# Kernel optimization log

Hardware: AMD Instinct MI355X
Metric: run time of the kernel (lower is better)

The kernel has to match this reference:

```python
import jax, jax.numpy as jnp
import numpy as np

N = 40000      # option nodes
E = 320000     # edges per edge type (avg in-degree 8)
NT = 3         # edge types
L = 3          # message-passing layers
D = 128        # node_dim
HID = 256      # hidden_dim
H = 4          # attention heads
C = HID // H   # per-head channels


def _ln(x, g, b):
    m = x.mean(-1, keepdims=True)
    v = ((x - m) ** 2).mean(-1, keepdims=True)
    return g * (x - m) * jax.lax.rsqrt(v + 1e-5) + b


def _gelu(x):
    return jax.nn.gelu(x, approximate=False)  # torch default = exact erf GELU


def _gat(h, src, dst, W, a_src, a_dst, bias):
    # PyG GATConv: shared src/dst linear, add_self_loops=False, eval (no dropout)
    xp = (h @ W).reshape(N, H, C)                      # (N,H,C)
    e = jax.nn.leaky_relu((xp * a_src).sum(-1)[src] + (xp * a_dst).sum(-1)[dst], 0.2)  # (E,H)
    emax = jax.ops.segment_max(e, dst, num_segments=N)
    emax = jnp.where(jnp.isfinite(emax), emax, 0.0)    # nodes with no in-edges
    ex = jnp.exp(e - emax[dst])
    den = jax.ops.segment_sum(ex, dst, num_segments=N)
    alpha = ex / (den[dst] + 1e-16)                    # segment softmax over incoming edges
    out = jax.ops.segment_sum(alpha[:, :, None] * xp[src], dst, num_segments=N)
    return out.reshape(N, HID) + bias


def _glorot(key, shape):
    fan_in = shape[-2] if len(shape) > 1 else shape[-1]
    return jax.random.normal(key, shape, jnp.float32) / np.sqrt(fan_in)


def setup_inputs() -> dict:
    key = jax.random.key(0)
    ks = jax.random.split(key, 16)
    return {
        "x": jax.random.normal(ks[0], (N, D), jnp.float32),
        "liquidity_features": jax.random.normal(ks[1], (N, 4), jnp.float32),
        "edge_index": jax.random.randint(ks[2], (NT, 2, E), 0, N, jnp.int32),
        "edge_weight": jax.random.uniform(ks[3], (NT, E), jnp.float32),
        "in_W": _glorot(ks[4], (D, HID)), "in_b": jnp.zeros((HID,)),
        "in_g": jnp.ones((HID,)), "in_bb": jnp.zeros((HID,)),
        "gat_W": _glorot(ks[5], (L, NT, HID, HID)),
        "gat_asrc": _glorot(ks[6], (L, NT, H, C)) * 0.1,
        "gat_adst": _glorot(ks[7], (L, NT, H, C)) * 0.1,
        "gat_bias": jnp.zeros((L, NT, HID)),
        "ln_g": jnp.ones((L, HID)), "ln_b": jnp.zeros((L, HID)),
        "gate_W": _glorot(ks[8], (HID + 4, 1)), "gate_b": jnp.zeros((1,)),
        "out_W1": _glorot(ks[9], (HID, HID)), "out_b1": jnp.zeros((HID,)),
        "out_g": jnp.ones((HID,)), "out_bb": jnp.zeros((HID,)),
        "out_W2": _glorot(ks[10], (HID, D)), "out_b2": jnp.zeros((D,)),
        "ro_W1": _glorot(ks[11], (D, HID)), "ro_b1": jnp.zeros((HID,)),
        "ro_W2": _glorot(ks[12], (HID, HID)), "ro_b2": jnp.zeros((HID,)),
    }


def reference(x, liquidity_features, edge_index, edge_weight, in_W, in_b, in_g, in_bb,
              gat_W, gat_asrc, gat_adst, gat_bias, ln_g, ln_b, gate_W, gate_b,
              out_W1, out_b1, out_g, out_bb, out_W2, out_b2,
              ro_W1, ro_b1, ro_W2, ro_b2):
    h = _gelu(_ln(x @ in_W + in_b, in_g, in_bb))  # input_proj
    # incoming edge-weight gate (static graph -> identical every layer)
    wsum = jnp.zeros((N,), x.dtype)
    deg = jnp.zeros((N,), x.dtype)
    for t in range(NT):
        dst = edge_index[t, 1]
        wsum = wsum.at[dst].add(edge_weight[t])
        deg = deg.at[dst].add(1.0)
    ewg = (0.5 + jax.nn.sigmoid(wsum / jnp.maximum(deg, 1.0)))[:, None]  # (N,1)
    layer_outputs = []
    for i in range(L):
        agg = jnp.zeros((N, HID), x.dtype)  # HeteroConv aggr='sum'
        for t in range(NT):
            agg = agg + _gat(h, edge_index[t, 0], edge_index[t, 1],
                             gat_W[i, t], gat_asrc[i, t], gat_adst[i, t], gat_bias[i, t])
        gate = jax.nn.sigmoid(jnp.concatenate([agg, liquidity_features], -1) @ gate_W + gate_b)
        hn = (gate * agg + (1.0 - gate) * h) * ewg   # liquidity gate + edge-weight gate
        h = _gelu(_ln(hn + h, ln_g[i], ln_b[i]))     # residual + LayerNorm + GELU
        layer_outputs.append(h)
    ho = _gelu(_ln(h @ out_W1 + out_b1, out_g, out_bb)) @ out_W2 + out_b2  # (N,D)
    surf = _gelu(ho.mean(0) @ ro_W1 + ro_b1) @ ro_W2 + ro_b2               # (HID,)
    return (ho, surf, *layer_outputs)
```

## Files before the change

kernel.cpp:

```cpp
#include <hip/hip_runtime.h>
#include <hip/hip_bf16.h>
#include <math.h>

#define NN 40000
#define EE 320000
#define NT 3
#define LL 3
#define DD 128
#define HID 256
#define NH 4
#define CC 64
#define NP 768

typedef __attribute__((ext_vector_type(8))) short short8;
typedef __attribute__((ext_vector_type(4))) float f32x4;

__device__ __forceinline__ float gelu_f(float x) {
    return 0.5f * x * (1.0f + erff(x * 0.70710678118654752440f));
}
__device__ __forceinline__ float lrelu_f(float x) {
    return x > 0.0f ? x : 0.2f * x;
}
__device__ __forceinline__ float bf2f(unsigned short u) {
    unsigned int x = ((unsigned int)u) << 16;
    float f;
    __builtin_memcpy(&f, &x, 4);
    return f;
}
__device__ __forceinline__ unsigned short f2bf(float f) {
    __hip_bfloat16 h = __float2bfloat16(f);
    unsigned short u;
    __builtin_memcpy(&u, &h, 2);
    return u;
}
__device__ __forceinline__ void gload16(const void* g, void* l) {
    __builtin_amdgcn_global_load_lds(
        (const __attribute__((address_space(1))) unsigned int*)g,
        (__attribute__((address_space(3))) unsigned int*)l, 16, 0, 0);
}

__global__ void wconv_k(const float* __restrict__ W, unsigned short* __restrict__ Wt,
                        int nmat, int K, int N) {
    int idx = blockIdx.x * 256 + threadIdx.x;
    int tot = nmat * K * N;
    if (idx >= tot) return;
    int m = idx / (K * N);
    int rem = idx - m * (K * N);
    int k = rem / N;
    int n = rem - k * N;
    Wt[(size_t)m * K * N + (size_t)n * K + k] = f2bf(W[idx]);
}

__global__ void xconv_k(const float* __restrict__ x, unsigned short* __restrict__ xb) {
    int idx = blockIdx.x * 256 + threadIdx.x;
    if (idx >= NN * DD / 4) return;
    float4 v = *reinterpret_cast<const float4*>(&x[(size_t)idx * 4]);
    ushort4 o;
    o.x = f2bf(v.x); o.y = f2bf(v.y); o.z = f2bf(v.z); o.w = f2bf(v.w);
    *reinterpret_cast<ushort4*>(&xb[(size_t)idx * 4]) = o;
}

__global__ __launch_bounds__(256) void gemm_mfma_k(const unsigned short* __restrict__ A,
                                                   const unsigned short* __restrict__ Bt,
                                                   const float* __restrict__ bias,
                                                   float* __restrict__ Cf,
                                                   unsigned short* __restrict__ Cb,
                                                   int M, int K, int N) {
    __shared__ __align__(16) short As[128 * 32];
    __shared__ __align__(16) short Bs[128 * 32];
    int bm = blockIdx.y * 128, bn = blockIdx.x * 128;
    int tid = threadIdx.x;
    int lane = tid & 63, w = tid >> 6;
    int wr = w >> 1, wc = w & 1;
    int l16 = lane & 15, kgrp = lane >> 4;
    f32x4 acc[4][4] = {};
    for (int k0 = 0; k0 < K; k0 += 32) {
        #pragma unroll
        for (int i = 0; i < 2; i++) {
            int chunk = (i * 4 + w) * 64 + lane;
            int row = chunk >> 2, kq = chunk & 3;
            int grow = bm + row; if (grow > M - 1) grow = M - 1;
            gload16(A + (size_t)grow * K + k0 + kq * 8, &As[(i * 4 + w) * 512]);
        }
        #pragma unroll
        for (int i = 0; i < 2; i++) {
            int chunk = (i * 4 + w) * 64 + lane;
            int row = chunk >> 2, kq = chunk & 3;
            gload16(Bt + (size_t)(bn + row) * K + k0 + kq * 8, &Bs[(i * 4 + w) * 512]);
        }
        __syncthreads();
        short8 af[4], bf[4];
        #pragma unroll
        for (int mi = 0; mi < 4; mi++) {
            int row = wr * 64 + mi * 16 + l16;
            af[mi] = *reinterpret_cast<const short8*>(&As[row * 32 + kgrp * 8]);
        }
        #pragma unroll
        for (int ni = 0; ni < 4; ni++) {
            int nrow = wc * 64 + ni * 16 + l16;
            bf[ni] = *reinterpret_cast<const short8*>(&Bs[nrow * 32 + kgrp * 8]);
        }
        #pragma unroll
        for (int mi = 0; mi < 4; mi++)
            #pragma unroll
            for (int ni = 0; ni < 4; ni++)
                acc[mi][ni] = __builtin_amdgcn_mfma_f32_16x16x32_bf16(af[mi], bf[ni], acc[mi][ni], 0, 0, 0);
        __syncthreads();
    }
    #pragma unroll
    for (int mi = 0; mi < 4; mi++) {
        #pragma unroll
        for (int r = 0; r < 4; r++) {
            int row = bm + wr * 64 + mi * 16 + (lane >> 4) * 4 + r;
            if (row < M) {
                #pragma unroll
                for (int ni = 0; ni < 4; ni++) {
                    int col = bn + wc * 64 + ni * 16 + l16;
                    float v = acc[mi][ni][r] + (bias ? bias[col] : 0.0f);
                    if (Cf) Cf[(size_t)row * N + col] = v;
                    if (Cb) Cb[(size_t)row * N + col] = f2bf(v);
                }
            }
        }
    }
}

__global__ __launch_bounds__(256) void ln_gelu_k(const float* __restrict__ y,
                                                 const float* __restrict__ g,
                                                 const float* __restrict__ b,
                                                 float* __restrict__ outf,
                                                 unsigned short* __restrict__ outb) {
    int n = blockIdx.x * 4 + (threadIdx.x >> 6);
    int lane = threadIdx.x & 63;
    float4 v = *reinterpret_cast<const float4*>(&y[(size_t)n * HID + lane * 4]);
    float s = v.x + v.y + v.z + v.w;
    float q = v.x * v.x + v.y * v.y + v.z * v.z + v.w * v.w;
    #pragma unroll
    for (int o = 32; o; o >>= 1) { s += __shfl_xor(s, o); q += __shfl_xor(q, o); }
    float mean = s * (1.0f / HID);
    float var = q * (1.0f / HID) - mean * mean;
    float rs = rsqrtf(var + 1e-5f);
    float4 gv = *reinterpret_cast<const float4*>(&g[lane * 4]);
    float4 bv = *reinterpret_cast<const float4*>(&b[lane * 4]);
    float o0 = gelu_f(gv.x * (v.x - mean) * rs + bv.x);
    float o1 = gelu_f(gv.y * (v.y - mean) * rs + bv.y);
    float o2 = gelu_f(gv.z * (v.z - mean) * rs + bv.z);
    float o3 = gelu_f(gv.w * (v.w - mean) * rs + bv.w);
    if (outf) {
        float4 ov = {o0, o1, o2, o3};
        *reinterpret_cast<float4*>(&outf[(size_t)n * HID + lane * 4]) = ov;
    }
    ushort4 ob;
    ob.x = f2bf(o0); ob.y = f2bf(o1); ob.z = f2bf(o2); ob.w = f2bf(o3);
    *reinterpret_cast<ushort4*>(&outb[(size_t)n * HID + lane * 4]) = ob;
}

__global__ void hist_k(const int* __restrict__ ei, int* __restrict__ cnt) {
    int gid = blockIdx.x * 256 + threadIdx.x;
    if (gid >= NT * EE) return;
    int t = gid / EE, e = gid - t * EE;
    int dst = ei[(size_t)t * 2 * EE + EE + e];
    atomicAdd(&cnt[t * NN + dst], 1);
}

__global__ __launch_bounds__(256) void scan1_k(const int* __restrict__ cnt, int* __restrict__ bsum, int n) {
    int i = blockIdx.x * 256 + threadIdx.x;
    int v = (i < n) ? cnt[i] : 0;
    #pragma unroll
    for (int o = 32; o; o >>= 1) v += __shfl_xor(v, o);
    __shared__ int s4[4];
    if ((threadIdx.x & 63) == 0) s4[threadIdx.x >> 6] = v;
    __syncthreads();
    if (threadIdx.x == 0) bsum[blockIdx.x] = s4[0] + s4[1] + s4[2] + s4[3];
}

__global__ __launch_bounds__(512) void scan2_k(const int* __restrict__ bsum, int* __restrict__ boff, int nb) {
    __shared__ int sh[512];
    int t = threadIdx.x;
    int v = (t < nb) ? bsum[t] : 0;
    sh[t] = v;
    __syncthreads();
    for (int o = 1; o < 512; o <<= 1) {
        int tv = (t >= o) ? sh[t - o] : 0;
        __syncthreads();
        sh[t] += tv;
        __syncthreads();
    }
    if (t < nb) boff[t] = sh[t] - v;
}

__global__ __launch_bounds__(256) void scan3_k(const int* __restrict__ cnt, const int* __restrict__ boff,
                                               int* __restrict__ roff, int n) {
    int i = blockIdx.x * 256 + threadIdx.x;
    int lane = threadIdx.x & 63, w = threadIdx.x >> 6;
    int v = (i < n) ? cnt[i] : 0;
    int s = v;
    #pragma unroll
    for (int o = 1; o < 64; o <<= 1) {
        int tv = __shfl_up(s, o);
        if (lane >= o) s += tv;
    }
    __shared__ int ws_[4];
    if (lane == 63) ws_[w] = s;
    __syncthreads();
    int add = 0;
    for (int k = 0; k < 4; k++) if (k < w) add += ws_[k];
    int incl = s + add + boff[blockIdx.x];
    if (i < n) roff[i] = incl - v;
    if (i == n - 1) roff[n] = incl;
}

__global__ void scatter_k(const int* __restrict__ ei, const float* __restrict__ ew,
                          const int* __restrict__ roff, int* __restrict__ cur,
                          int* __restrict__ csr_src, float* __restrict__ csr_ew) {
    int gid = blockIdx.x * 256 + threadIdx.x;
    if (gid >= NT * EE) return;
    int t = gid / EE, e = gid - t * EE;
    int src = ei[(size_t)t * 2 * EE + e];
    int dst = ei[(size_t)t * 2 * EE + EE + e];
    int pos = roff[t * NN + dst] + atomicAdd(&cur[t * NN + dst], 1);
    csr_src[pos] = src;
    csr_ew[pos] = ew[gid];
}

__global__ void ewg_kernel(const int* __restrict__ roff, const float* __restrict__ csr_ew,
                           float* __restrict__ ewg) {
    int n = blockIdx.x * 256 + threadIdx.x;
    if (n >= NN) return;
    float ws = 0.0f;
    int dg = 0;
    for (int t = 0; t < NT; t++) {
        int beg = roff[t * NN + n], end = roff[t * NN + n + 1];
        dg += end - beg;
        for (int e = beg; e < end; e++) ws += csr_ew[e];
    }
    float m = dg > 1 ? (float)dg : 1.0f;
    float z = ws / m;
    ewg[n] = 0.5f + 1.0f / (1.0f + __expf(-z));
}

__global__ __launch_bounds__(256) void compute_s_k(const unsigned short* __restrict__ xpa,
                                                   const float* __restrict__ asrc,
                                                   const float* __restrict__ adst,
                                                   float* __restrict__ ss,
                                                   float* __restrict__ sd) {
    int t = blockIdx.x / (NN / 4);
    int node = (blockIdx.x % (NN / 4)) * 4 + (threadIdx.x >> 6);
    int lane = threadIdx.x & 63;
    ushort4 v = *reinterpret_cast<const ushort4*>(&xpa[(size_t)node * NP + t * HID + lane * 4]);
    float4 av = *reinterpret_cast<const float4*>(&asrc[t * HID + lane * 4]);
    float4 dv = *reinterpret_cast<const float4*>(&adst[t * HID + lane * 4]);
    float x0 = bf2f(v.x), x1 = bf2f(v.y), x2 = bf2f(v.z), x3 = bf2f(v.w);
    float p = x0 * av.x + x1 * av.y + x2 * av.z + x3 * av.w;
    float q = x0 * dv.x + x1 * dv.y + x2 * dv.z + x3 * dv.w;
    #pragma unroll
    for (int o = 8; o; o >>= 1) { p += __shfl_xor(p, o); q += __shfl_xor(q, o); }
    if ((lane & 15) == 0) {
        ss[((size_t)t * NN + node) * NH + (lane >> 4)] = p;
        sd[((size_t)t * NN + node) * NH + (lane >> 4)] = q;
    }
}

__global__ __launch_bounds__(256) void layer_k(const unsigned short* __restrict__ xpa,
                                               const float* __restrict__ ss,
                                               const float* __restrict__ sd,
                                               const int* __restrict__ roff,
                                               const int* __restrict__ rsrc,
                                               const float* __restrict__ gatb,
                                               const float* __restrict__ hin,
                                               const float* __restrict__ liq,
                                               const float* __restrict__ gW,
                                               const float* __restrict__ gb,
                                               const float* __restrict__ ewg,
                                               const float* __restrict__ lg,
                                               const float* __restrict__ lb,
                                               float* __restrict__ hout,
                                               unsigned short* __restrict__ houtb) {
    int node = blockIdx.x * 4 + (threadIdx.x >> 6);
    int lane = threadIdx.x & 63;
    int h = lane >> 4;
    float agg0 = 0, agg1 = 0, agg2 = 0, agg3 = 0;
    #pragma unroll
    for (int t = 0; t < NT; t++) {
        int beg = roff[t * NN + node], end = roff[t * NN + node + 1];
        if (beg == end) continue;
        float sdh = sd[((size_t)t * NN + node) * NH + h];
        float m = -1e30f, den = 0, a0 = 0, a1 = 0, a2 = 0, a3 = 0;
        int s_n = rsrc[beg];
        float sv_n = ss[((size_t)t * NN + s_n) * NH + h];
        ushort4 xr_n = *reinterpret_cast<const ushort4*>(&xpa[(size_t)s_n * NP + t * HID + lane * 4]);
        for (int e = beg; e < end; e++) {
            float sv_c = sv_n;
            ushort4 xr_c = xr_n;
            if (e + 1 < end) {
                int sn = rsrc[e + 1];
                sv_n = ss[((size_t)t * NN + sn) * NH + h];
                xr_n = *reinterpret_cast<const ushort4*>(&xpa[(size_t)sn * NP + t * HID + lane * 4]);
            }
            float sc = lrelu_f(sv_c + sdh);
            float wg;
            if (sc > m) {
                float r = __expf(m - sc);
                den *= r; a0 *= r; a1 *= r; a2 *= r; a3 *= r;
                m = sc;
                wg = 1.0f;
            } else {
                wg = __expf(sc - m);
            }
            den += wg;
            a0 += wg * bf2f(xr_c.x);
            a1 += wg * bf2f(xr_c.y);
            a2 += wg * bf2f(xr_c.z);
            a3 += wg * bf2f(xr_c.w);
        }
        float inv = 1.0f / (den + 1e-16f);
        agg0 += a0 * inv; agg1 += a1 * inv; agg2 += a2 * inv; agg3 += a3 * inv;
    }
    float4 bb0 = *reinterpret_cast<const float4*>(&gatb[lane * 4]);
    float4 bb1 = *reinterpret_cast<const float4*>(&gatb[HID + lane * 4]);
    float4 bb2 = *reinterpret_cast<const float4*>(&gatb[2 * HID + lane * 4]);
    agg0 += bb0.x + bb1.x + bb2.x;
    agg1 += bb0.y + bb1.y + bb2.y;
    agg2 += bb0.z + bb1.z + bb2.z;
    agg3 += bb0.w + bb1.w + bb2.w;
    float4 gwv = *reinterpret_cast<const float4*>(&gW[lane * 4]);
    float part = agg0 * gwv.x + agg1 * gwv.y + agg2 * gwv.z + agg3 * gwv.w;
    if (lane < 4) part += liq[node * 4 + lane] * gW[HID + lane];
    #pragma unroll
    for (int o = 32; o; o >>= 1) part += __shfl_xor(part, o);
    float gate = 1.0f / (1.0f + __expf(-(part + gb[0])));
    float eg = ewg[node];
    float4 hh = *reinterpret_cast<const float4*>(&hin[(size_t)node * HID + lane * 4]);
    float v0 = (gate * agg0 + (1.0f - gate) * hh.x) * eg + hh.x;
    float v1 = (gate * agg1 + (1.0f - gate) * hh.y) * eg + hh.y;
    float v2 = (gate * agg2 + (1.0f - gate) * hh.z) * eg + hh.z;
    float v3 = (gate * agg3 + (1.0f - gate) * hh.w) * eg + hh.w;
    float s = v0 + v1 + v2 + v3;
    float q = v0 * v0 + v1 * v1 + v2 * v2 + v3 * v3;
    #pragma unroll
    for (int o = 32; o; o >>= 1) { s += __shfl_xor(s, o); q += __shfl_xor(q, o); }
    float mean = s * (1.0f / HID);
    float var = q * (1.0f / HID) - mean * mean;
    float rs = rsqrtf(var + 1e-5f);
    float4 lgv = *reinterpret_cast<const float4*>(&lg[lane * 4]);
    float4 lbv = *reinterpret_cast<const float4*>(&lb[lane * 4]);
    float o0 = gelu_f(lgv.x * (v0 - mean) * rs + lbv.x);
    float o1 = gelu_f(lgv.y * (v1 - mean) * rs + lbv.y);
    float o2 = gelu_f(lgv.z * (v2 - mean) * rs + lbv.z);
    float o3 = gelu_f(lgv.w * (v3 - mean) * rs + lbv.w);
    float4 ov = {o0, o1, o2, o3};
    *reinterpret_cast<float4*>(&hout[(size_t)node * HID + lane * 4]) = ov;
    ushort4 ob;
    ob.x = f2bf(o0); ob.y = f2bf(o1); ob.z = f2bf(o2); ob.w = f2bf(o3);
    *reinterpret_cast<ushort4*>(&houtb[(size_t)node * HID + lane * 4]) = ob;
}

__global__ __launch_bounds__(128) void colpart_k(const float* __restrict__ ho,
                                                 float* __restrict__ part) {
    int c = threadIdx.x, b = blockIdx.x;
    float s = 0.0f;
    for (int r = b; r < NN; r += 256) s += ho[(size_t)r * DD + c];
    part[b * DD + c] = s;
}

__global__ __launch_bounds__(256) void readout_k(const float* __restrict__ part,
                                                 const float* __restrict__ W1,
                                                 const float* __restrict__ b1,
                                                 const float* __restrict__ W2,
                                                 const float* __restrict__ b2,
                                                 float* __restrict__ surf) {
    __shared__ float m[DD];
    __shared__ float a1[HID];
    int t = threadIdx.x;
    if (t < DD) {
        float s = 0.0f;
        for (int b = 0; b < 256; b++) s += part[b * DD + t];
        m[t] = s / (float)NN;
    }
    __syncthreads();
    float s1 = b1[t];
    for (int k = 0; k < DD; k++) s1 += m[k] * W1[k * HID + t];
    a1[t] = gelu_f(s1);
    __syncthreads();
    float s2 = b2[t];
    for (int k = 0; k < HID; k++) s2 += a1[k] * W2[k * HID + t];
    surf[t] = s2;
}

extern "C" void kernel_launch(void* const* d_in, const int* in_sizes, int n_in,
                              void* d_out, int out_size, void* d_ws, size_t ws_size,
                              hipStream_t stream) {
    const float* x       = (const float*)d_in[0];
    const float* liq     = (const float*)d_in[1];
    const int*   ei      = (const int*)d_in[2];
    const float* ew      = (const float*)d_in[3];
    const float* in_W    = (const float*)d_in[4];
    const float* in_b    = (const float*)d_in[5];
    const float* in_g    = (const float*)d_in[6];
    const float* in_bb   = (const float*)d_in[7];
    const float* gat_W   = (const float*)d_in[8];
    const float* gat_as  = (const float*)d_in[9];
    const float* gat_ad  = (const float*)d_in[10];
    const float* gat_b   = (const float*)d_in[11];
    const float* ln_g    = (const float*)d_in[12];
    const float* ln_b    = (const float*)d_in[13];
    const float* gate_W  = (const float*)d_in[14];
    const float* gate_b  = (const float*)d_in[15];
    const float* out_W1  = (const float*)d_in[16];
    const float* out_b1  = (const float*)d_in[17];
    const float* out_g   = (const float*)d_in[18];
    const float* out_bb  = (const float*)d_in[19];
    const float* out_W2  = (const float*)d_in[20];
    const float* out_b2  = (const float*)d_in[21];
    const float* ro_W1   = (const float*)d_in[22];
    const float* ro_b1   = (const float*)d_in[23];
    const float* ro_W2   = (const float*)d_in[24];
    const float* ro_b2   = (const float*)d_in[25];

    float* out = (float*)d_out;
    float* out_ho   = out;
    float* out_surf = out + (size_t)NN * DD;
    float* out_h[3];
    out_h[0] = out_surf + HID;
    out_h[1] = out_h[0] + (size_t)NN * HID;
    out_h[2] = out_h[1] + (size_t)NN * HID;

    char* wsb = (char*)d_ws;
    size_t off = 0;
    auto alloc = [&](size_t bytes) { char* p = wsb + off; off += (bytes + 255) & ~(size_t)255; return p; };
    unsigned short* xpa = (unsigned short*)alloc((size_t)NN * NP * 2);
    float* Cf32 = (float*)xpa;
    unsigned short* xb = xpa + (size_t)NN * 512;
    unsigned short* hb = (unsigned short*)alloc((size_t)NN * HID * 2);
    unsigned short* Wt_in  = (unsigned short*)alloc((size_t)DD * HID * 2);
    unsigned short* Wt_gat = (unsigned short*)alloc((size_t)LL * NT * HID * HID * 2);
    unsigned short* Wt_o1  = (unsigned short*)alloc((size_t)HID * HID * 2);
    unsigned short* Wt_o2  = (unsigned short*)alloc((size_t)HID * DD * 2);
    size_t cew_b = (size_t)NT * EE * 4;
    size_t cnt_b = (size_t)NT * NN * 4;
    char* R = alloc(cew_b + cnt_b + 2 * 2048 * 4);
    float* cew = (float*)R;
    int* cnt   = (int*)(R + cew_b);
    int* bsum  = (int*)(R + cew_b + cnt_b);
    int* boff  = bsum + 2048;
    float* ss  = (float*)R;
    float* sd  = ss + (size_t)NT * NN * NH;
    int* roff  = (int*)alloc(((size_t)NT * NN + 1) * 4);
    int* rsrc  = (int*)alloc((size_t)NT * EE * 4);
    float* ewg = (float*)alloc((size_t)NN * 4);
    float* cpart = (float*)alloc((size_t)256 * DD * 4);

    const int NSC = (NT * NN + 255) / 256;

    wconv_k<<<(DD * HID + 255) / 256, 256, 0, stream>>>(in_W, Wt_in, 1, DD, HID);
    wconv_k<<<(LL * NT * HID * HID + 255) / 256, 256, 0, stream>>>(gat_W, Wt_gat, LL * NT, HID, HID);
    wconv_k<<<(HID * HID + 255) / 256, 256, 0, stream>>>(out_W1, Wt_o1, 1, HID, HID);
    wconv_k<<<(HID * DD + 255) / 256, 256, 0, stream>>>(out_W2, Wt_o2, 1, HID, DD);
    xconv_k<<<(NN * DD / 4 + 255) / 256, 256, 0, stream>>>(x, xb);

    gemm_mfma_k<<<dim3(HID / 128, (NN + 127) / 128), 256, 0, stream>>>(
        xb, Wt_in, in_b, Cf32, nullptr, NN, DD, HID);
    ln_gelu_k<<<NN / 4, 256, 0, stream>>>(Cf32, in_g, in_bb, out_h[0], hb);

    hipMemsetAsync(cnt, 0, cnt_b, stream);
    hist_k<<<(NT * EE + 255) / 256, 256, 0, stream>>>(ei, cnt);
    scan1_k<<<NSC, 256, 0, stream>>>(cnt, bsum, NT * NN);
    scan2_k<<<1, 512, 0, stream>>>(bsum, boff, NSC);
    scan3_k<<<NSC, 256, 0, stream>>>(cnt, boff, roff, NT * NN);
    hipMemsetAsync(cnt, 0, cnt_b, stream);
    scatter_k<<<(NT * EE + 255) / 256, 256, 0, stream>>>(ei, ew, roff, cnt, rsrc, cew);
    ewg_kernel<<<(NN + 255) / 256, 256, 0, stream>>>(roff, cew, ewg);

    const float* hin_f = out_h[0];
    for (int i = 0; i < LL; i++) {
        gemm_mfma_k<<<dim3(NP / 128, (NN + 127) / 128), 256, 0, stream>>>(
            hb, Wt_gat + (size_t)i * NP * HID, nullptr, nullptr, xpa, NN, HID, NP);
        compute_s_k<<<NT * (NN / 4), 256, 0, stream>>>(
            xpa, gat_as + (size_t)i * NT * HID, gat_ad + (size_t)i * NT * HID, ss, sd);
        layer_k<<<NN / 4, 256, 0, stream>>>(
            xpa, ss, sd, roff, rsrc, gat_b + (size_t)i * NT * HID,
            hin_f, liq, gate_W, gate_b, ewg, ln_g + i * HID, ln_b + i * HID,
            out_h[i], hb);
        hin_f = out_h[i];
    }

    gemm_mfma_k<<<dim3(HID / 128, (NN + 127) / 128), 256, 0, stream>>>(
        hb, Wt_o1, out_b1, Cf32, nullptr, NN, HID, HID);
    ln_gelu_k<<<NN / 4, 256, 0, stream>>>(Cf32, out_g, out_bb, nullptr, hb);
    gemm_mfma_k<<<dim3(DD / 128, (NN + 127) / 128), 256, 0, stream>>>(
        hb, Wt_o2, out_b2, out_ho, nullptr, NN, HID, DD);

    colpart_k<<<256, 128, 0, stream>>>(out_ho, cpart);
    readout_k<<<1, 256, 0, stream>>>(cpart, ro_W1, ro_b1, ro_W2, ro_b2, out_surf);
}
```

Before: 851.2 us.

## Persistent grid-stride layer kernel, drop online-softmax max, read residual from bf16

```diff
diff --git a/kernel.cpp b/kernel.cpp
--- a/kernel.cpp
+++ b/kernel.cpp
@@ -11,6 +11,7 @@
 #define NH 4
 #define CC 64
 #define NP 768
+#define LGRID 2048
 
 typedef __attribute__((ext_vector_type(8))) short short8;
 typedef __attribute__((ext_vector_type(4))) float f32x4;
@@ -267,7 +268,6 @@
                                                const int* __restrict__ roff,
                                                const int* __restrict__ rsrc,
                                                const float* __restrict__ gatb,
-                                               const float* __restrict__ hin,
                                                const float* __restrict__ liq,
                                                const float* __restrict__ gW,
                                                const float* __restrict__ gb,
@@ -275,84 +275,83 @@
                                                const float* __restrict__ lg,
                                                const float* __restrict__ lb,
                                                float* __restrict__ hout,
-                                               unsigned short* __restrict__ houtb) {
-    int node = blockIdx.x * 4 + (threadIdx.x >> 6);
+                                               unsigned short* __restrict__ hb) {
+    int wid = blockIdx.x * 4 + (threadIdx.x >> 6);
     int lane = threadIdx.x & 63;
     int h = lane >> 4;
-    float agg0 = 0, agg1 = 0, agg2 = 0, agg3 = 0;
-    #pragma unroll
-    for (int t = 0; t < NT; t++) {
-        int beg = roff[t * NN + node], end = roff[t * NN + node + 1];
-        if (beg == end) continue;
-        float sdh = sd[((size_t)t * NN + node) * NH + h];
-        float m = -1e30f, den = 0, a0 = 0, a1 = 0, a2 = 0, a3 = 0;
-        int s_n = rsrc[beg];
-        float sv_n = ss[((size_t)t * NN + s_n) * NH + h];
-        ushort4 xr_n = *reinterpret_cast<const ushort4*>(&xpa[(size_t)s_n * NP + t * HID + lane * 4]);
-        for (int e = beg; e < end; e++) {
-            float sv_c = sv_n;
-            ushort4 xr_c = xr_n;
-            if (e + 1 < end) {
-                int sn = rsrc[e + 1];
-                sv_n = ss[((size_t)t * NN + sn) * NH + h];
-                xr_n = *reinterpret_cast<const ushort4*>(&xpa[(size_t)sn * NP + t * HID + lane * 4]);
-            }
-            float sc = lrelu_f(sv_c + sdh);
-            float wg;
-            if (sc > m) {
-                float r = __expf(m - sc);
-                den *= r; a0 *= r; a1 *= r; a2 *= r; a3 *= r;
-                m = sc;
-                wg = 1.0f;
-            } else {
-                wg = __expf(sc - m);
-            }
-            den += wg;
-            a0 += wg * bf2f(xr_c.x);
-            a1 += wg * bf2f(xr_c.y);
-            a2 += wg * bf2f(xr_c.z);
-            a3 += wg * bf2f(xr_c.w);
-        }
-        float inv = 1.0f / (den + 1e-16f);
-        agg0 += a0 * inv; agg1 += a1 * inv; agg2 += a2 * inv; agg3 += a3 * inv;
-    }
+    const int nw = LGRID * 4;
     float4 bb0 = *reinterpret_cast<const float4*>(&gatb[lane * 4]);
     float4 bb1 = *reinterpret_cast<const float4*>(&gatb[HID + lane * 4]);
     float4 bb2 = *reinterpret_cast<const float4*>(&gatb[2 * HID + lane * 4]);
-    agg0 += bb0.x + bb1.x + bb2.x;
-    agg1 += bb0.y + bb1.y + bb2.y;
-    agg2 += bb0.z + bb1.z + bb2.z;
-    agg3 += bb0.w + bb1.w + bb2.w;
+    float bs0 = bb0.x + bb1.x + bb2.x;
+    float bs1 = bb0.y + bb1.y + bb2.y;
+    float bs2 = bb0.z + bb1.z + bb2.z;
+    float bs3 = bb0.w + bb1.w + bb2.w;
     float4 gwv = *reinterpret_cast<const float4*>(&gW[lane * 4]);
-    float part = agg0 * gwv.x + agg1 * gwv.y + agg2 * gwv.z + agg3 * gwv.w;
-    if (lane < 4) part += liq[node * 4 + lane] * gW[HID + lane];
-    #pragma unroll
-    for (int o = 32; o; o >>= 1) part += __shfl_xor(part, o);
-    float gate = 1.0f / (1.0f + __expf(-(part + gb[0])));
-    float eg = ewg[node];
-    float4 hh = *reinterpret_cast<const float4*>(&hin[(size_t)node * HID + lane * 4]);
-    float v0 = (gate * agg0 + (1.0f - gate) * hh.x) * eg + hh.x;
-    float v1 = (gate * agg1 + (1.0f - gate) * hh.y) * eg + hh.y;
-    float v2 = (gate * agg2 + (1.0f - gate) * hh.z) * eg + hh.z;
-    float v3 = (gate * agg3 + (1.0f - gate) * hh.w) * eg + hh.w;
-    float s = v0 + v1 + v2 + v3;
-    float q = v0 * v0 + v1 * v1 + v2 * v2 + v3 * v3;
-    #pragma unroll
-    for (int o = 32; o; o >>= 1) { s += __shfl_xor(s, o); q += __shfl_xor(q, o); }
-    float mean = s * (1.0f / HID);
-    float var = q * (1.0f / HID) - mean * mean;
-    float rs = rsqrtf(var + 1e-5f);
+    float gwl = (lane < 4) ? gW[HID + lane] : 0.0f;
+    float gb0 = gb[0];
     float4 lgv = *reinterpret_cast<const float4*>(&lg[lane * 4]);
     float4 lbv = *reinterpret_cast<const float4*>(&lb[lane * 4]);
-    float o0 = gelu_f(lgv.x * (v0 - mean) * rs + lbv.x);
-    float o1 = gelu_f(lgv.y * (v1 - mean) * rs + lbv.y);
-    float o2 = gelu_f(lgv.z * (v2 - mean) * rs + lbv.z);
-    float o3 = gelu_f(lgv.w * (v3 - mean) * rs + lbv.w);
-    float4 ov = {o0, o1, o2, o3};
-    *reinterpret_cast<float4*>(&hout[(size_t)node * HID + lane * 4]) = ov;
-    ushort4 ob;
-    ob.x = f2bf(o0); ob.y = f2bf(o1); ob.z = f2bf(o2); ob.w = f2bf(o3);
-    *reinterpret_cast<ushort4*>(&houtb[(size_t)node * HID + lane * 4]) = ob;
+
+    for (int node = wid; node < NN; node += nw) {
+        float agg0 = 0, agg1 = 0, agg2 = 0, agg3 = 0;
+        #pragma unroll
+        for (int t = 0; t < NT; t++) {
+            int base = t * NN;
+            int beg = roff[base + node], end = roff[base + node + 1];
+            if (beg == end) continue;
+            float sdh = sd[(size_t)(base + node) * NH + h];
+            float den = 0, a0 = 0, a1 = 0, a2 = 0, a3 = 0;
+            int sp = rsrc[beg];
+            float svp = ss[(size_t)(base + sp) * NH + h];
+            ushort4 xrp = *reinterpret_cast<const ushort4*>(&xpa[(size_t)sp * NP + t * HID + lane * 4]);
+            for (int e = beg; e < end; e++) {
+                float sv_c = svp;
+                ushort4 xr_c = xrp;
+                int en = (e + 1 < end) ? (e + 1) : e;
+                int sn = rsrc[en];
+                svp = ss[(size_t)(base + sn) * NH + h];
+                xrp = *reinterpret_cast<const ushort4*>(&xpa[(size_t)sn * NP + t * HID + lane * 4]);
+                float wg = __expf(lrelu_f(sv_c + sdh));
+                den += wg;
+                a0 += wg * bf2f(xr_c.x);
+                a1 += wg * bf2f(xr_c.y);
+                a2 += wg * bf2f(xr_c.z);
+                a3 += wg * bf2f(xr_c.w);
+            }
+            float inv = 1.0f / (den + 1e-16f);
+            agg0 += a0 * inv; agg1 += a1 * inv; agg2 += a2 * inv; agg3 += a3 * inv;
+        }
+        agg0 += bs0; agg1 += bs1; agg2 += bs2; agg3 += bs3;
+        float part = agg0 * gwv.x + agg1 * gwv.y + agg2 * gwv.z + agg3 * gwv.w;
+        if (lane < 4) part += liq[node * 4 + lane] * gwl;
+        #pragma unroll
+        for (int o = 32; o; o >>= 1) part += __shfl_xor(part, o);
+        float gate = 1.0f / (1.0f + __expf(-(part + gb0)));
+        float eg = ewg[node];
+        ushort4 hu = *reinterpret_cast<const ushort4*>(&hb[(size_t)node * HID + lane * 4]);
+        float h0 = bf2f(hu.x), h1 = bf2f(hu.y), h2 = bf2f(hu.z), h3 = bf2f(hu.w);
+        float v0 = (gate * agg0 + (1.0f - gate) * h0) * eg + h0;
+        float v1 = (gate * agg1 + (1.0f - gate) * h1) * eg + h1;
+        float v2 = (gate * agg2 + (1.0f - gate) * h2) * eg + h2;
+        float v3 = (gate * agg3 + (1.0f - gate) * h3) * eg + h3;
+        float s = v0 + v1 + v2 + v3;
+        float q = v0 * v0 + v1 * v1 + v2 * v2 + v3 * v3;
+        #pragma unroll
+        for (int o = 32; o; o >>= 1) { s += __shfl_xor(s, o); q += __shfl_xor(q, o); }
+        float mean = s * (1.0f / HID);
+        float var = q * (1.0f / HID) - mean * mean;
+        float rs = rsqrtf(var + 1e-5f);
+        float o0 = gelu_f(lgv.x * (v0 - mean) * rs + lbv.x);
+        float o1 = gelu_f(lgv.y * (v1 - mean) * rs + lbv.y);
+        float o2 = gelu_f(lgv.z * (v2 - mean) * rs + lbv.z);
+        float o3 = gelu_f(lgv.w * (v3 - mean) * rs + lbv.w);
+        float4 ov = {o0, o1, o2, o3};
+        *reinterpret_cast<float4*>(&hout[(size_t)node * HID + lane * 4]) = ov;
+        ushort4 ob;
+        ob.x = f2bf(o0); ob.y = f2bf(o1); ob.z = f2bf(o2); ob.w = f2bf(o3);
+        *reinterpret_cast<ushort4*>(&hb[(size_t)node * HID + lane * 4]) = ob;
+    }
 }
 
 __global__ __launch_bounds__(128) void colpart_k(const float* __restrict__ ho,
@@ -460,7 +459,7 @@
 
     gemm_mfma_k<<<dim3(HID / 128, (NN + 127) / 128), 256, 0, stream>>>(
         xb, Wt_in, in_b, Cf32, nullptr, NN, DD, HID);
-    ln_gelu_k<<<NN / 4, 256, 0, stream>>>(Cf32, in_g, in_bb, out_h[0], hb);
+    ln_gelu_k<<<NN / 4, 256, 0, stream>>>(Cf32, in_g, in_bb, nullptr, hb);
 
     hipMemsetAsync(cnt, 0, cnt_b, stream);
     hist_k<<<(NT * EE + 255) / 256, 256, 0, stream>>>(ei, cnt);
@@ -471,17 +470,15 @@
     scatter_k<<<(NT * EE + 255) / 256, 256, 0, stream>>>(ei, ew, roff, cnt, rsrc, cew);
     ewg_kernel<<<(NN + 255) / 256, 256, 0, stream>>>(roff, cew, ewg);
 
-    const float* hin_f = out_h[0];
     for (int i = 0; i < LL; i++) {
         gemm_mfma_k<<<dim3(NP / 128, (NN + 127) / 128), 256, 0, stream>>>(
             hb, Wt_gat + (size_t)i * NP * HID, nullptr, nullptr, xpa, NN, HID, NP);
         compute_s_k<<<NT * (NN / 4), 256, 0, stream>>>(
             xpa, gat_as + (size_t)i * NT * HID, gat_ad + (size_t)i * NT * HID, ss, sd);
-        layer_k<<<NN / 4, 256, 0, stream>>>(
+        layer_k<<<LGRID, 256, 0, stream>>>(
             xpa, ss, sd, roff, rsrc, gat_b + (size_t)i * NT * HID,
-            hin_f, liq, gate_W, gate_b, ewg, ln_g + i * HID, ln_b + i * HID,
+            liq, gate_W, gate_b, ewg, ln_g + i * HID, ln_b + i * HID,
             out_h[i], hb);
-        hin_f = out_h[i];
     }
 
     gemm_mfma_k<<<dim3(HID / 128, (NN + 127) / 128), 256, 0, stream>>>(
```

New measurement: 838.6 us. Within noise of the previous version (-1.5%).
